# Performance work log

Hardware: AMD Instinct MI355X
Metric: run time of the kernel (lower is better)

## Reference

```python
import jax, jax.numpy as jnp
import numpy as np

NUM_NODES = 1_000_000
HIDDEN = 256
NUM_GRAPHS = 1024


def setup_inputs() -> dict:
    key = jax.random.key(0)
    k_x, k_b, k_w1, k_b1, k_w2, k_b2 = jax.random.split(key, 6)
    x = jax.random.normal(k_x, (NUM_NODES, HIDDEN), dtype=jnp.float32)
    batch = jnp.sort(jax.random.randint(k_b, (NUM_NODES,), 0, NUM_GRAPHS, dtype=jnp.int64))
    h = HIDDEN // 2
    # torch Linear default init: U(-1/sqrt(fan_in), 1/sqrt(fan_in))
    s1 = 1.0 / np.sqrt(HIDDEN)
    s2 = 1.0 / np.sqrt(h)
    w1 = jax.random.uniform(k_w1, (HIDDEN, h), jnp.float32, -s1, s1)
    b1 = jax.random.uniform(k_b1, (h,), jnp.float32, -s1, s1)
    w2 = jax.random.uniform(k_w2, (h, 1), jnp.float32, -s2, s2)
    b2 = jax.random.uniform(k_b2, (1,), jnp.float32, -s2, s2)
    return {"x": x, "batch": batch, "w1": w1, "b1": b1, "w2": w2, "b2": b2}


def reference(x, batch, w1, b1, w2, b2):
    # attention MLP: Linear -> tanh -> Linear -> scalar score per node
    scores = (jnp.tanh(x @ w1 + b1) @ w2 + b2)[:, 0]  # [N]
    # segment softmax over nodes of each graph (numerically stable)
    seg_max = jax.ops.segment_max(scores, batch, num_segments=NUM_GRAPHS)  # [B]
    e = jnp.exp(scores - seg_max[batch])  # [N]
    denom = jax.ops.segment_sum(e, batch, num_segments=NUM_GRAPHS)  # [B]
    attn = e / denom[batch]  # [N]
    # attention-weighted scatter-add pooling -> [B, H]
    return jax.ops.segment_sum(x * attn[:, None], batch, num_segments=NUM_GRAPHS)
```

## Files before the change

### kernel.cpp

```cpp
#include <hip/hip_runtime.h>
#include <stdint.h>

#define N_NODES 1000000
#define HID 256
#define HH  128
#define NG  1024

typedef short short8v __attribute__((ext_vector_type(8)));
typedef float f32x4 __attribute__((ext_vector_type(4)));

__device__ __forceinline__ unsigned short f2bf(float f){
  unsigned u = __float_as_uint(f);
  u += 0x7FFFu + ((u >> 16) & 1u);
  return (unsigned short)(u >> 16);
}

__device__ __forceinline__ float fast_tanh(float v){
  float e = __expf(2.f * v);
  return 1.f - 2.f / (e + 1.f);
}

__global__ void k_prep(const float* __restrict__ w1, unsigned short* __restrict__ w1f){
  int s = blockIdx.x * blockDim.x + threadIdx.x;
  if (s >= 4096) return;
  int nt = s >> 9, rem = s & 511, ks = rem >> 6, lane = rem & 63;
  int q = lane >> 4, c = lane & 15;
  union { unsigned short u[8]; uint4 v; } tmp;
  for (int i = 0; i < 8; ++i){
    int k = ks * 32 + q * 8 + i;
    int n = nt * 16 + c;
    tmp.u[i] = f2bf(w1[k * HH + n]);
  }
  *(uint4*)(w1f + (size_t)s * 8) = tmp.v;
}

__global__ __launch_bounds__(256) void k_score(
    const float* __restrict__ x, const unsigned short* __restrict__ w1f,
    const float* __restrict__ b1, const float* __restrict__ w2,
    const float* __restrict__ b2, const int* __restrict__ batch,
    float* __restrict__ escore, float* __restrict__ denom, int num_tiles)
{
  __shared__ unsigned short w1s[32768];
  const int tid = threadIdx.x;
  for (int i = tid; i < 4096; i += 256)
    ((uint4*)w1s)[i] = ((const uint4*)w1f)[i];
  __syncthreads();

  const int wave = tid >> 6, lane = tid & 63;
  const int q = lane >> 4, col = lane & 15;

  float b1v[8], w2v[8];
  #pragma unroll
  for (int nt = 0; nt < 8; ++nt){
    int j = nt * 16 + col;
    b1v[nt] = b1[j];
    w2v[nt] = w2[j];
  }
  const float b2v = b2[0];

  for (int tile = blockIdx.x; tile < num_tiles; tile += gridDim.x){
    const int node0 = tile * 64 + wave * 16;
    f32x4 acc[8];
    #pragma unroll
    for (int nt = 0; nt < 8; ++nt) acc[nt] = (f32x4){0.f, 0.f, 0.f, 0.f};

    const float* xrow = x + (size_t)(node0 + col) * HID;
    #pragma unroll
    for (int ks = 0; ks < 8; ++ks){
      const float4* xp = (const float4*)(xrow + ks * 32 + q * 8);
      float4 xa = xp[0], xb = xp[1];
      short8v a;
      a[0] = (short)f2bf(xa.x); a[1] = (short)f2bf(xa.y);
      a[2] = (short)f2bf(xa.z); a[3] = (short)f2bf(xa.w);
      a[4] = (short)f2bf(xb.x); a[5] = (short)f2bf(xb.y);
      a[6] = (short)f2bf(xb.z); a[7] = (short)f2bf(xb.w);
      #pragma unroll
      for (int nt = 0; nt < 8; ++nt){
        short8v bfr = *(const short8v*)&w1s[(((size_t)nt * 8 + ks) * 64 + lane) * 8];
        acc[nt] = __builtin_amdgcn_mfma_f32_16x16x32_bf16(a, bfr, acc[nt], 0, 0, 0);
      }
    }
    float e_lane = 0.f;
    #pragma unroll
    for (int r = 0; r < 4; ++r){
      float p = 0.f;
      #pragma unroll
      for (int nt = 0; nt < 8; ++nt)
        p += fast_tanh(acc[nt][r] + b1v[nt]) * w2v[nt];
      p += __shfl_xor(p, 1);
      p += __shfl_xor(p, 2);
      p += __shfl_xor(p, 4);
      p += __shfl_xor(p, 8);
      if (col == r){
        float e = __expf(p + b2v);
        e_lane = e;
        escore[node0 + q * 4 + r] = e;
      }
    }
    int bfirst = batch[node0];
    int blast  = batch[node0 + 15];
    if (bfirst == blast){
      float s = e_lane;
      s += __shfl_xor(s, 1);  s += __shfl_xor(s, 2);
      s += __shfl_xor(s, 16); s += __shfl_xor(s, 32);
      s += __shfl_xor(s, 4);  s += __shfl_xor(s, 8);
      if (lane == 0) atomicAdd(&denom[bfirst], s);
    } else if (col < 4){
      int b = batch[node0 + q * 4 + col];
      atomicAdd(&denom[b], e_lane);
    }
  }
}

__global__ __launch_bounds__(256) void k_pool(
    const float* __restrict__ x, const int* __restrict__ batch,
    const float* __restrict__ escore, const float* __restrict__ denom,
    float* __restrict__ out)
{
  __shared__ float w_s[1024];
  __shared__ int b_s[1024];
  const int tid = threadIdx.x;
  const long base = (long)blockIdx.x * 1024;
  int cnt = (int)(N_NODES - base); if (cnt > 1024) cnt = 1024;
  for (int i = tid; i < cnt; i += 256){
    int b = batch[base + i];
    b_s[i] = b;
    w_s[i] = __fdividef(escore[base + i], denom[b]);
  }
  __syncthreads();

  const int g = tid >> 6;
  const int lane = tid & 63;
  const float4* xp = (const float4*)(x + base * HID) + lane;

  float4 acc = {0.f, 0.f, 0.f, 0.f};
  int cur = b_s[g];
  float4 xv = {0.f, 0.f, 0.f, 0.f};
  if (g < cnt) xv = xp[(long)g * (HID / 4)];
  for (int i = g; i < cnt; i += 4){
    int inext = i + 4;
    float4 xnext = {0.f, 0.f, 0.f, 0.f};
    if (inext < cnt) xnext = xp[(long)inext * (HID / 4)];
    int b = b_s[i];
    float w = w_s[i];
    if (b != cur){
      float* o = &out[(long)cur * HID + lane * 4];
      atomicAdd(o + 0, acc.x); atomicAdd(o + 1, acc.y);
      atomicAdd(o + 2, acc.z); atomicAdd(o + 3, acc.w);
      acc = (float4){0.f, 0.f, 0.f, 0.f};
      cur = b;
    }
    acc.x += w * xv.x; acc.y += w * xv.y;
    acc.z += w * xv.z; acc.w += w * xv.w;
    xv = xnext;
  }
  {
    float* o = &out[(long)cur * HID + lane * 4];
    atomicAdd(o + 0, acc.x); atomicAdd(o + 1, acc.y);
    atomicAdd(o + 2, acc.z); atomicAdd(o + 3, acc.w);
  }
}

extern "C" void kernel_launch(void* const* d_in, const int* in_sizes, int n_in,
                              void* d_out, int out_size, void* d_ws, size_t ws_size,
                              hipStream_t stream){
  const float* x     = (const float*)d_in[0];
  const int*   batch = (const int*)d_in[1];
  const float* w1    = (const float*)d_in[2];
  const float* b1    = (const float*)d_in[3];
  const float* w2    = (const float*)d_in[4];
  const float* b2    = (const float*)d_in[5];
  float* out = (float*)d_out;

  char* ws = (char*)d_ws;
  unsigned short* w1f = (unsigned short*)ws;
  float* escore = (float*)(ws + 65536);
  float* denom  = (float*)(ws + 65536 + 4000000);

  hipMemsetAsync(denom, 0, 4096, stream);
  hipMemsetAsync(d_out, 0, (size_t)out_size * sizeof(float), stream);

  k_prep<<<16, 256, 0, stream>>>(w1, w1f);
  k_score<<<2048, 256, 0, stream>>>(x, w1f, b1, w2, b2, batch, escore, denom, N_NODES / 64);
  k_pool<<<(N_NODES + 1023) / 1024, 256, 0, stream>>>(x, batch, escore, denom, out);
}
```

Measured before the change: 1.786 ms.

## Fuse score and pooling into one pass with LDS-staged x tiles

Merges the scoring MLP and the weighted segment pooling into a single kernel. Each block streams its chunk of x into double-buffered LDS with global_load_lds, computes scores with MFMA from register-resident W1 fragments, and accumulates exp(score)*x directly into out. Normalisation by the segment denominator is deferred to a small k_norm kernel, which removes the second full read of x and the escore buffer. The trade-offs are three block barriers per 32-node tile, fewer and longer-lived blocks, and higher LDS use per block.

```diff
diff --git a/kernel.cpp b/kernel.cpp
--- a/kernel.cpp
+++ b/kernel.cpp
@@ -5,9 +5,15 @@
 #define HID 256
 #define HH  128
 #define NG  1024
+#define TILE 32
+#define CHUNK 1984
+#define NBLOCKS ((N_NODES + CHUNK - 1) / CHUNK)
 
 typedef short short8v __attribute__((ext_vector_type(8)));
 typedef float f32x4 __attribute__((ext_vector_type(4)));
+
+#define GLOBAL_AS __attribute__((address_space(1)))
+#define LDS_AS    __attribute__((address_space(3)))
 
 __device__ __forceinline__ unsigned short f2bf(float f){
   unsigned u = __float_as_uint(f);
@@ -34,131 +40,151 @@
   *(uint4*)(w1f + (size_t)s * 8) = tmp.v;
 }
 
-__global__ __launch_bounds__(256) void k_score(
+__device__ __forceinline__ void stage_tile(const float* __restrict__ x, long node0,
+                                           float* lds_tile, int wave, int lane){
+  #pragma unroll
+  for (int rr = 0; rr < 8; ++rr){
+    int r = wave * 8 + rr;
+    const float* gp = x + (size_t)(node0 + r) * HID + ((lane ^ (r & 15)) << 2);
+    __builtin_amdgcn_global_load_lds(
+        (const GLOBAL_AS unsigned int*)gp,
+        (LDS_AS unsigned int*)(lds_tile + r * HID),
+        16, 0, 0);
+  }
+}
+
+__global__ __launch_bounds__(256, 2) void k_fused(
     const float* __restrict__ x, const unsigned short* __restrict__ w1f,
     const float* __restrict__ b1, const float* __restrict__ w2,
     const float* __restrict__ b2, const int* __restrict__ batch,
-    float* __restrict__ escore, float* __restrict__ denom, int num_tiles)
+    float* __restrict__ denom, float* __restrict__ out)
 {
-  __shared__ unsigned short w1s[32768];
+  __shared__ __align__(16) float xs[2][TILE * HID];
+  __shared__ int   b_all[CHUNK];
+  __shared__ float partial_s[4][TILE];
+  __shared__ float e_s[TILE];
+
   const int tid = threadIdx.x;
-  for (int i = tid; i < 4096; i += 256)
-    ((uint4*)w1s)[i] = ((const uint4*)w1f)[i];
-  __syncthreads();
+  const long base = (long)blockIdx.x * CHUNK;
+  if (base >= N_NODES) return;
+  long rem = (long)N_NODES - base;
+  const int nvalid = (rem < CHUNK) ? (int)rem : CHUNK;
+  const int ntiles = nvalid / TILE;
 
   const int wave = tid >> 6, lane = tid & 63;
   const int q = lane >> 4, col = lane & 15;
 
-  float b1v[8], w2v[8];
+  for (int i = tid; i < nvalid; i += 256) b_all[i] = batch[base + i];
+
+  short8v wf0[8], wf1[8];
   #pragma unroll
-  for (int nt = 0; nt < 8; ++nt){
-    int j = nt * 16 + col;
-    b1v[nt] = b1[j];
-    w2v[nt] = w2[j];
-  }
+  for (int ks = 0; ks < 8; ++ks){
+    int nt0 = wave * 2;
+    wf0[ks] = *(const short8v*)(w1f + (((size_t)nt0 * 8 + ks) * 64 + lane) * 8);
+    wf1[ks] = *(const short8v*)(w1f + ((((size_t)nt0 + 1) * 8 + ks) * 64 + lane) * 8);
+  }
+  float b1v0 = b1[wave * 32 + col],      w2v0 = w2[wave * 32 + col];
+  float b1v1 = b1[wave * 32 + 16 + col], w2v1 = w2[wave * 32 + 16 + col];
   const float b2v = b2[0];
 
-  for (int tile = blockIdx.x; tile < num_tiles; tile += gridDim.x){
-    const int node0 = tile * 64 + wave * 16;
-    f32x4 acc[8];
-    #pragma unroll
-    for (int nt = 0; nt < 8; ++nt) acc[nt] = (f32x4){0.f, 0.f, 0.f, 0.f};
-
-    const float* xrow = x + (size_t)(node0 + col) * HID;
+  stage_tile(x, base, &xs[0][0], wave, lane);
+
+  float accp = 0.f;
+  int curg = batch[base];
+
+  for (int t = 0; t < ntiles; ++t){
+    const int par = t & 1;
+    __syncthreads();
+
+    if (t + 1 < ntiles)
+      stage_tile(x, base + (long)(t + 1) * TILE, &xs[par ^ 1][0], wave, lane);
+
+    const float* xb = &xs[par][0];
+
+    f32x4 acc00 = {0.f,0.f,0.f,0.f}, acc01 = {0.f,0.f,0.f,0.f};
+    f32x4 acc10 = {0.f,0.f,0.f,0.f}, acc11 = {0.f,0.f,0.f,0.f};
     #pragma unroll
     for (int ks = 0; ks < 8; ++ks){
-      const float4* xp = (const float4*)(xrow + ks * 32 + q * 8);
-      float4 xa = xp[0], xb = xp[1];
-      short8v a;
-      a[0] = (short)f2bf(xa.x); a[1] = (short)f2bf(xa.y);
-      a[2] = (short)f2bf(xa.z); a[3] = (short)f2bf(xa.w);
-      a[4] = (short)f2bf(xb.x); a[5] = (short)f2bf(xb.y);
-      a[6] = (short)f2bf(xb.z); a[7] = (short)f2bf(xb.w);
+      const int k16 = ks * 8 + q * 2;
       #pragma unroll
-      for (int nt = 0; nt < 8; ++nt){
-        short8v bfr = *(const short8v*)&w1s[(((size_t)nt * 8 + ks) * 64 + lane) * 8];
-        acc[nt] = __builtin_amdgcn_mfma_f32_16x16x32_bf16(a, bfr, acc[nt], 0, 0, 0);
-      }
-    }
-    float e_lane = 0.f;
+      for (int rg = 0; rg < 2; ++rg){
+        const int R  = rg * 16 + col;
+        const int sw = R & 15;
+        f32x4 xa = *(const f32x4*)(xb + R * HID + ((k16 ^ sw) << 2));
+        f32x4 xc = *(const f32x4*)(xb + R * HID + (((k16 + 1) ^ sw) << 2));
+        short8v a;
+        a[0] = (short)f2bf(xa[0]); a[1] = (short)f2bf(xa[1]);
+        a[2] = (short)f2bf(xa[2]); a[3] = (short)f2bf(xa[3]);
+        a[4] = (short)f2bf(xc[0]); a[5] = (short)f2bf(xc[1]);
+        a[6] = (short)f2bf(xc[2]); a[7] = (short)f2bf(xc[3]);
+        if (rg == 0){
+          acc00 = __builtin_amdgcn_mfma_f32_16x16x32_bf16(a, wf0[ks], acc00, 0, 0, 0);
+          acc01 = __builtin_amdgcn_mfma_f32_16x16x32_bf16(a, wf1[ks], acc01, 0, 0, 0);
+        } else {
+          acc10 = __builtin_amdgcn_mfma_f32_16x16x32_bf16(a, wf0[ks], acc10, 0, 0, 0);
+          acc11 = __builtin_amdgcn_mfma_f32_16x16x32_bf16(a, wf1[ks], acc11, 0, 0, 0);
+        }
+      }
+    }
     #pragma unroll
-    for (int r = 0; r < 4; ++r){
-      float p = 0.f;
+    for (int rg = 0; rg < 2; ++rg){
       #pragma unroll
-      for (int nt = 0; nt < 8; ++nt)
-        p += fast_tanh(acc[nt][r] + b1v[nt]) * w2v[nt];
-      p += __shfl_xor(p, 1);
-      p += __shfl_xor(p, 2);
-      p += __shfl_xor(p, 4);
-      p += __shfl_xor(p, 8);
-      if (col == r){
-        float e = __expf(p + b2v);
-        e_lane = e;
-        escore[node0 + q * 4 + r] = e;
-      }
-    }
-    int bfirst = batch[node0];
-    int blast  = batch[node0 + 15];
-    if (bfirst == blast){
-      float s = e_lane;
-      s += __shfl_xor(s, 1);  s += __shfl_xor(s, 2);
-      s += __shfl_xor(s, 16); s += __shfl_xor(s, 32);
-      s += __shfl_xor(s, 4);  s += __shfl_xor(s, 8);
-      if (lane == 0) atomicAdd(&denom[bfirst], s);
-    } else if (col < 4){
-      int b = batch[node0 + q * 4 + col];
-      atomicAdd(&denom[b], e_lane);
-    }
-  }
-}
-
-__global__ __launch_bounds__(256) void k_pool(
-    const float* __restrict__ x, const int* __restrict__ batch,
-    const float* __restrict__ escore, const float* __restrict__ denom,
-    float* __restrict__ out)
-{
-  __shared__ float w_s[1024];
-  __shared__ int b_s[1024];
-  const int tid = threadIdx.x;
-  const long base = (long)blockIdx.x * 1024;
-  int cnt = (int)(N_NODES - base); if (cnt > 1024) cnt = 1024;
-  for (int i = tid; i < cnt; i += 256){
-    int b = batch[base + i];
-    b_s[i] = b;
-    w_s[i] = __fdividef(escore[base + i], denom[b]);
-  }
-  __syncthreads();
-
-  const int g = tid >> 6;
-  const int lane = tid & 63;
-  const float4* xp = (const float4*)(x + base * HID) + lane;
-
-  float4 acc = {0.f, 0.f, 0.f, 0.f};
-  int cur = b_s[g];
-  float4 xv = {0.f, 0.f, 0.f, 0.f};
-  if (g < cnt) xv = xp[(long)g * (HID / 4)];
-  for (int i = g; i < cnt; i += 4){
-    int inext = i + 4;
-    float4 xnext = {0.f, 0.f, 0.f, 0.f};
-    if (inext < cnt) xnext = xp[(long)inext * (HID / 4)];
-    int b = b_s[i];
-    float w = w_s[i];
-    if (b != cur){
-      float* o = &out[(long)cur * HID + lane * 4];
-      atomicAdd(o + 0, acc.x); atomicAdd(o + 1, acc.y);
-      atomicAdd(o + 2, acc.z); atomicAdd(o + 3, acc.w);
-      acc = (float4){0.f, 0.f, 0.f, 0.f};
-      cur = b;
-    }
-    acc.x += w * xv.x; acc.y += w * xv.y;
-    acc.z += w * xv.z; acc.w += w * xv.w;
-    xv = xnext;
-  }
-  {
-    float* o = &out[(long)cur * HID + lane * 4];
-    atomicAdd(o + 0, acc.x); atomicAdd(o + 1, acc.y);
-    atomicAdd(o + 2, acc.z); atomicAdd(o + 3, acc.w);
-  }
+      for (int r = 0; r < 4; ++r){
+        float a0 = (rg == 0) ? acc00[r] : acc10[r];
+        float a1 = (rg == 0) ? acc01[r] : acc11[r];
+        float p = fast_tanh(a0 + b1v0) * w2v0 + fast_tanh(a1 + b1v1) * w2v1;
+        p += __shfl_xor(p, 1); p += __shfl_xor(p, 2);
+        p += __shfl_xor(p, 4); p += __shfl_xor(p, 8);
+        if (col == r) partial_s[wave][rg * 16 + q * 4 + r] = p;
+      }
+    }
+    __syncthreads();
+
+    if (tid < TILE){
+      float pt = partial_s[0][tid] + partial_s[1][tid]
+               + partial_s[2][tid] + partial_s[3][tid];
+      float e = __expf(pt + b2v);
+      e_s[tid] = e;
+      int b  = b_all[t * TILE + tid];
+      int b0 = b_all[t * TILE];
+      int bl = b_all[t * TILE + TILE - 1];
+      if (b0 == bl){
+        float s = e;
+        s += __shfl_xor(s, 1);  s += __shfl_xor(s, 2);
+        s += __shfl_xor(s, 4);  s += __shfl_xor(s, 8);
+        s += __shfl_xor(s, 16);
+        if (tid == 0) atomicAdd(&denom[b0], s);
+      } else {
+        atomicAdd(&denom[b], e);
+      }
+    }
+    __syncthreads();
+
+    {
+      const int chi = tid >> 2, clo = tid & 3;
+      #pragma unroll 8
+      for (int i = 0; i < TILE; ++i){
+        int b   = b_all[t * TILE + i];
+        float e = e_s[i];
+        float xv = xb[i * HID + ((chi ^ (i & 15)) << 2) + clo];
+        if (b != curg){
+          atomicAdd(&out[(size_t)curg * HID + tid], accp);
+          accp = 0.f;
+          curg = b;
+        }
+        accp += e * xv;
+      }
+    }
+  }
+  atomicAdd(&out[(size_t)curg * HID + tid], accp);
+}
+
+__global__ void k_norm(float* __restrict__ out, const float* __restrict__ denom){
+  int g = blockIdx.x, c = threadIdx.x;
+  float d = denom[g];
+  size_t idx = (size_t)g * HID + c;
+  float o = out[idx];
+  out[idx] = (d > 0.f) ? __fdividef(o, d) : 0.f;
 }
 
 extern "C" void kernel_launch(void* const* d_in, const int* in_sizes, int n_in,
@@ -174,13 +200,12 @@
 
   char* ws = (char*)d_ws;
   unsigned short* w1f = (unsigned short*)ws;
-  float* escore = (float*)(ws + 65536);
-  float* denom  = (float*)(ws + 65536 + 4000000);
+  float* denom = (float*)(ws + 65536);
 
   hipMemsetAsync(denom, 0, 4096, stream);
   hipMemsetAsync(d_out, 0, (size_t)out_size * sizeof(float), stream);
 
   k_prep<<<16, 256, 0, stream>>>(w1, w1f);
-  k_score<<<2048, 256, 0, stream>>>(x, w1f, b1, w2, b2, batch, escore, denom, N_NODES / 64);
-  k_pool<<<(N_NODES + 1023) / 1024, 256, 0, stream>>>(x, batch, escore, denom, out);
-}
+  k_fused<<<NBLOCKS, 256, 0, stream>>>(x, w1f, b1, w2, b2, batch, denom, out);
+  k_norm<<<NG, 256, 0, stream>>>(out, denom);
+}
```

After: 1.485 ms. -16.9%, faster.
